# Kernel tuning notes

Hardware: AMD Instinct MI355X
Metric: run time of the kernel (lower is better)

Reference implementation:

```python
import jax, jax.numpy as jnp
import numpy as np

D_MODEL = 1024
N_HEADS = 16
HEAD_DIM = D_MODEL // N_HEADS
BATCH = 2
SEQ = 2048


def setup_inputs() -> dict:
    key = jax.random.key(0)
    ks = jax.random.split(key, 7)
    s = 1.0 / np.sqrt(D_MODEL)
    return {
        "x": jax.random.normal(ks[0], (BATCH, SEQ, D_MODEL), dtype=jnp.float32),
        "Wq": jax.random.normal(ks[1], (D_MODEL, D_MODEL), dtype=jnp.float32) * s,
        "Wk": jax.random.normal(ks[2], (D_MODEL, D_MODEL), dtype=jnp.float32) * s,
        "Wv": jax.random.normal(ks[3], (D_MODEL, D_MODEL), dtype=jnp.float32) * s,
        "Wo": jax.random.normal(ks[4], (D_MODEL, D_MODEL), dtype=jnp.float32) * s,
        "Wg": jax.random.normal(ks[5], (D_MODEL, D_MODEL), dtype=jnp.float32) * s,
        "bg": jnp.zeros((D_MODEL,), dtype=jnp.float32),
    }


def _rope_cos_sin(seq_len, head_dim, dtype):
    half = head_dim // 2
    inv_freq = 1.0 / (10000.0 ** (jnp.arange(half, dtype=jnp.float32) / half))
    freqs = jnp.arange(seq_len, dtype=jnp.float32)[:, None] * inv_freq[None, :]  # (S, half)
    emb = jnp.concatenate([freqs, freqs], axis=-1)  # (S, head_dim)
    return jnp.cos(emb).astype(dtype), jnp.sin(emb).astype(dtype)


def _rotate_half(x):
    half = x.shape[-1] // 2
    return jnp.concatenate([-x[..., half:], x[..., :half]], axis=-1)


def reference(x, Wq, Wk, Wv, Wo, Wg, bg):
    bsz, seq_len, d_model = x.shape
    # projections (torch Linear: x @ W.T)
    q = jnp.einsum('bsd,ed->bse', x, Wq).reshape(bsz, seq_len, N_HEADS, HEAD_DIM).transpose(0, 2, 1, 3)
    k = jnp.einsum('bsd,ed->bse', x, Wk).reshape(bsz, seq_len, N_HEADS, HEAD_DIM).transpose(0, 2, 1, 3)
    v = jnp.einsum('bsd,ed->bse', x, Wv).reshape(bsz, seq_len, N_HEADS, HEAD_DIM).transpose(0, 2, 1, 3)
    cos, sin = _rope_cos_sin(seq_len, HEAD_DIM, x.dtype)  # (S, hd)
    cos = cos[None, None]
    sin = sin[None, None]
    q = q * cos + _rotate_half(q) * sin
    k = k * cos + _rotate_half(k) * sin
    scores = jnp.einsum('bhqd,bhkd->bhqk', q, k) / jnp.sqrt(jnp.asarray(HEAD_DIM, x.dtype))
    causal = jnp.triu(jnp.full((seq_len, seq_len), -jnp.inf, dtype=x.dtype), k=1)
    scores = scores + causal
    probs = jax.nn.softmax(scores, axis=-1)
    attn = jnp.einsum('bhqk,bhkd->bhqd', probs, v)  # (B,H,S,hd)
    attn = attn.transpose(0, 2, 1, 3).reshape(bsz, seq_len, d_model)
    out = jnp.einsum('bsd,ed->bse', attn, Wo)
    gate = jax.nn.sigmoid(jnp.einsum('bsd,ed->bse', out, Wg) + bg)
    return out * gate
```

## Files before the change

### kernel.cpp

```cpp
#include <hip/hip_runtime.h>

#define DM 1024
#define NH 16
#define HD 64
#define BATCH 2
#define SEQ 2048
#define MROWS (BATCH*SEQ)

typedef unsigned short u16;
typedef unsigned long long u64;
typedef __bf16 bf16x8 __attribute__((ext_vector_type(8)));
typedef float f32x4 __attribute__((ext_vector_type(4)));
typedef unsigned int u32x4 __attribute__((ext_vector_type(4)));
typedef unsigned int __attribute__((address_space(1))) as1_uint;
typedef unsigned int __attribute__((address_space(3))) as3_uint;

__device__ __forceinline__ u16 f2bf(float f) {
  unsigned u = __builtin_bit_cast(unsigned, f);
  u += 0x7fffu + ((u >> 16) & 1u);
  return (u16)(u >> 16);
}
__device__ __forceinline__ float bf2f(u16 h) {
  return __builtin_bit_cast(float, ((unsigned)h) << 16);
}
__device__ __forceinline__ bf16x8 ld8(const u16* p) {
  return __builtin_bit_cast(bf16x8, *reinterpret_cast<const u32x4*>(p));
}
__device__ __forceinline__ void gl_lds16(const u16* g, void* lds) {
  __builtin_amdgcn_global_load_lds((const as1_uint*)(const void*)g,
                                   (as3_uint*)lds, 16, 0, 0);
}
__device__ __forceinline__ unsigned pk2(float a, float b) {
  return __builtin_amdgcn_perm(__builtin_bit_cast(unsigned, a),
                               __builtin_bit_cast(unsigned, b), 0x07060302u);
}

__global__ void convall_kernel(const float* __restrict__ x,
                               const float* __restrict__ w0, const float* __restrict__ w1,
                               const float* __restrict__ w2, const float* __restrict__ w3,
                               const float* __restrict__ w4, u16* __restrict__ out) {
  const size_t NX = (size_t)MROWS * DM;
  size_t i = ((size_t)blockIdx.x * 256 + threadIdx.x) * 4;
  const float* src;
  size_t off;
  if (i < NX) { src = x; off = i; }
  else {
    size_t j = i - NX;
    int wsel = (int)(j >> 20);
    off = j & ((1u << 20) - 1);
    src = (wsel == 0) ? w0 : (wsel == 1) ? w1 : (wsel == 2) ? w2 : (wsel == 3) ? w3 : w4;
  }
  f32x4 v = *reinterpret_cast<const f32x4*>(src + off);
  out[i + 0] = f2bf(v[0]);
  out[i + 1] = f2bf(v[1]);
  out[i + 2] = f2bf(v[2]);
  out[i + 3] = f2bf(v[3]);
}

__global__ void tab_kernel(float* __restrict__ tab) {
  int t = blockIdx.x * 256 + threadIdx.x;
  if (t >= SEQ * 32) return;
  int s = t >> 5, i = t & 31;
  float inv = powf(10000.0f, -(float)i / 32.0f);
  float f = (float)s * inv;
  tab[s * 64 + i] = cosf(f);
  tab[s * 64 + 32 + i] = sinf(f);
}

template <int MODE>
__global__ __launch_bounds__(256) void gemm_bt(
    const u16* __restrict__ A, const u16* __restrict__ B,
    u16* __restrict__ Cbf, float* __restrict__ Cf,
    const float* __restrict__ bias, const float* __restrict__ mult,
    int M, int N, int K, size_t bz, size_t cz) {
  B += blockIdx.z * bz;
  u16* Cb = Cbf + blockIdx.z * cz;
  const int gx = gridDim.x;
  {
    int nwg = gx * gridDim.y;
    int flat = blockIdx.y * gx + blockIdx.x;
    flat = (flat & 7) * (nwg >> 3) + (flat >> 3);
    const int bx = flat % gx, by = flat / gx;
    A += (size_t)by * 128 * K;
    B += (size_t)bx * 64 * K;
    Cb += (size_t)by * 128 * N + bx * 64;
    if constexpr (MODE != 0) Cf += (size_t)by * 128 * N + bx * 64;
    if constexpr (MODE == 2) { bias += bx * 64; mult += (size_t)by * 128 * N + bx * 64; }
  }
  const int t = threadIdx.x, w = t >> 6;
  const int l = t & 63;
  const int wr = w >> 1, wc = w & 1;
  const int lr = l & 15, lg = l >> 4;
  __shared__ __align__(16) u16 As[128 * 32];
  __shared__ __align__(16) u16 Bs[64 * 32];
  f32x4 acc[4][2] = {};
  const int srow = t >> 2;
  const int sc8 = (t & 3) * 8;
  const u16* gA = A + (size_t)srow * K + sc8;
  const u16* gB = B + (size_t)srow * K + sc8;
  char* lA = (char*)As + w * 1024;
  char* lB = (char*)Bs + w * 1024;
  const size_t rstep = (size_t)64 * K;

  for (int kt = 0; kt < K; kt += 32) {
    gl_lds16(gA + kt, lA);
    gl_lds16(gA + kt + rstep, lA + 4096);
    gl_lds16(gB + kt, lB);
    __syncthreads();
    bf16x8 af[4], bfr[2];
#pragma unroll
    for (int i = 0; i < 4; ++i)
      af[i] = ld8(&As[(wr * 64 + i * 16 + lr) * 32 + lg * 8]);
#pragma unroll
    for (int i = 0; i < 2; ++i)
      bfr[i] = ld8(&Bs[(wc * 32 + i * 16 + lr) * 32 + lg * 8]);
#pragma unroll
    for (int mi = 0; mi < 4; ++mi)
#pragma unroll
      for (int ni = 0; ni < 2; ++ni)
        acc[mi][ni] = __builtin_amdgcn_mfma_f32_16x16x32_bf16(af[mi], bfr[ni], acc[mi][ni], 0, 0, 0);
    __syncthreads();
  }
#pragma unroll
  for (int mi = 0; mi < 4; ++mi)
#pragma unroll
    for (int ni = 0; ni < 2; ++ni)
#pragma unroll
      for (int r = 0; r < 4; ++r) {
        int row = wr * 64 + mi * 16 + lg * 4 + r;
        int col = wc * 32 + ni * 16 + lr;
        size_t idx = (size_t)row * N + col;
        float v = acc[mi][ni][r];
        if constexpr (MODE == 0) {
          Cb[idx] = f2bf(v);
        } else if constexpr (MODE == 1) {
          Cf[idx] = v;
          Cb[idx] = f2bf(v);
        } else {
          float g = 1.0f / (1.0f + __expf(-(v + bias[col])));
          Cf[idx] = mult[idx] * g;
        }
      }
}

__global__ void rope_kernel(const u16* __restrict__ Qin, const u16* __restrict__ Kin,
                            u16* __restrict__ Qr, u16* __restrict__ Kr,
                            const float* __restrict__ tab) {
  int t = blockIdx.x * 256 + threadIdx.x;
  int i = t & 31;
  int s = (t >> 5) & (SEQ - 1);
  int bh = t >> 16;
  if (bh >= BATCH * NH) return;
  int b = bh >> 4, h = bh & 15;
  size_t ib = ((size_t)(b * SEQ + s)) * DM + h * 64;
  size_t ob = ((size_t)bh * SEQ + s) * 64;
  float c = tab[s * 64 + i], sn = tab[s * 64 + 32 + i];
  float q1 = bf2f(Qin[ib + i]), q2 = bf2f(Qin[ib + 32 + i]);
  float k1 = bf2f(Kin[ib + i]), k2 = bf2f(Kin[ib + 32 + i]);
  Qr[ob + i] = f2bf(q1 * c - q2 * sn);
  Qr[ob + 32 + i] = f2bf(q2 * c + q1 * sn);
  Kr[ob + i] = f2bf(k1 * c - k2 * sn);
  Kr[ob + 32 + i] = f2bf(k2 * c + k1 * sn);
}

__global__ __launch_bounds__(256) void vtrans_kernel(const u16* __restrict__ Vin,
                                                     u16* __restrict__ Vt) {
  const int s0 = blockIdx.x * 64;
  const int bh = blockIdx.y;
  const int b = bh >> 4, h = bh & 15;
  const int t = threadIdx.x;
  __shared__ __align__(16) u16 T[64][72];
  const int row = t >> 3, col = (t & 7) * 8;
#pragma unroll
  for (int p = 0; p < 2; ++p) {
    int r = p * 32 + row;
    *reinterpret_cast<u32x4*>(&T[r][col]) =
        *reinterpret_cast<const u32x4*>(&Vin[(size_t)(b * SEQ + s0 + r) * DM + h * 64 + col]);
  }
  __syncthreads();
  const size_t ob = (size_t)bh * 64 * SEQ;
#pragma unroll
  for (int p = 0; p < 2; ++p) {
    int dr = p * 32 + row;
    u16 tmp[8];
#pragma unroll
    for (int j = 0; j < 8; ++j) tmp[j] = T[col + j][dr];
    *reinterpret_cast<u32x4*>(&Vt[ob + (size_t)dr * SEQ + s0 + col]) =
        *reinterpret_cast<u32x4*>(tmp);
  }
}

__global__ __launch_bounds__(256) void attn_kernel(
    const u16* __restrict__ Q, const u16* __restrict__ K, const u16* __restrict__ Vt,
    u16* __restrict__ O) {
  const int qb_raw = blockIdx.x;
  const int bh_raw = blockIdx.y;
  const int xs = qb_raw & 7, hi = qb_raw >> 3;
  const int lo = bh_raw & 15, rr = bh_raw >> 4;
  const int bh = xs * 4 + (lo & 3);
  const int q0i = hi + 2 * (lo >> 2);
  const int qb = rr ? (15 - q0i) : q0i;

  const int t = threadIdx.x, w = t >> 6, l = t & 63;
  const int lr = l & 15, lg = l >> 4;
  const int qw0 = qb * 128 + w * 32;
  const size_t base = (size_t)bh * SEQ * 64;
  const size_t vbase = (size_t)bh * 64 * SEQ;
  __shared__ __align__(16) u16 Ks[2][64 * 64];
  __shared__ __align__(16) u16 Vs[2][64 * 64];
  __shared__ __align__(16) u16 Ps[4][2][1024];

  bf16x8 qf[2][2];
#pragma unroll
  for (int qs = 0; qs < 2; ++qs) {
    const u16* qp = &Q[base + (size_t)(qw0 + qs * 16 + lr) * 64 + lg * 8];
    qf[qs][0] = ld8(qp);
    qf[qs][1] = ld8(qp + 32);
  }

  f32x4 oacc[2][4] = {};
  float l_run[2] = {0.0f, 0.0f};

  const int nt = (qb + 1) * 2;
  const int srow = t >> 3, sc16 = t & 7;
  const int lo0 = srow * 128 + ((sc16 * 16) ^ ((srow & 7) << 4));
  const int lo1 = lo0 + 4096;
  const u16* Kg = K + base + sc16 * 8;
  const u16* Vg = Vt + vbase + sc16 * 8;
  u32x4 rg[4];

#define LOADG(tile) do { const int kv_ = (tile) * 64;                     \
    rg[0] = *(const u32x4*)(Kg + (size_t)(kv_ + srow) * 64);              \
    rg[1] = *(const u32x4*)(Kg + (size_t)(kv_ + srow + 32) * 64);         \
    rg[2] = *(const u32x4*)(Vg + (size_t)srow * SEQ + kv_);               \
    rg[3] = *(const u32x4*)(Vg + (size_t)(srow + 32) * SEQ + kv_); } while (0)

#define WRITEL(tile) do { char* kb_ = (char*)Ks[(tile) & 1];              \
    char* vb_ = (char*)Vs[(tile) & 1];                                    \
    *(u32x4*)(kb_ + lo0) = rg[0]; *(u32x4*)(kb_ + lo1) = rg[1];           \
    *(u32x4*)(vb_ + lo0) = rg[2]; *(u32x4*)(vb_ + lo1) = rg[3]; } while (0)

  LOADG(0);
  WRITEL(0);
  __syncthreads();

  for (int tk = 0; tk < nt; ++tk) {
    const int cur = tk & 1;
    const int kv0 = tk * 64;
    if (tk + 1 < nt) LOADG(tk + 1);
    const char* kb = (const char*)Ks[cur];
    const char* vb = (const char*)Vs[cur];
    if (kv0 <= qw0 + 31) {
      bf16x8 kf[4][2];
      const int swk = (lr & 7) << 4;
#pragma unroll
      for (int h = 0; h < 4; ++h) {
        const char* rp = kb + (h * 16 + lr) * 128;
        kf[h][0] = *(const bf16x8*)(rp + ((lg * 16) ^ swk));
        kf[h][1] = *(const bf16x8*)(rp + ((64 + lg * 16) ^ swk));
      }
      const int qslo = (kv0 <= qw0 + 15) ? 0 : 1;
      const int swz = (lr & 7) << 4;
#pragma unroll
      for (int qs = 0; qs < 2; ++qs) {
        if (qs < qslo) continue;
        const int qs0 = qw0 + qs * 16;
        f32x4 st[4];
#pragma unroll
        for (int h = 0; h < 4; ++h) {
          f32x4 z = {};
          z = __builtin_amdgcn_mfma_f32_16x16x32_bf16(kf[h][0], qf[qs][0], z, 0, 0, 0);
          z = __builtin_amdgcn_mfma_f32_16x16x32_bf16(kf[h][1], qf[qs][1], z, 0, 0, 0);
          st[h] = z;
        }
        float pv[4][4];
#pragma unroll
        for (int h = 0; h < 4; ++h)
#pragma unroll
          for (int r = 0; r < 4; ++r)
            pv[h][r] = fmaf(st[h][r], 0.1803368801f, -12.0f);
        if (kv0 + 63 > qs0) {
#pragma unroll
          for (int h = 0; h < 4; ++h)
#pragma unroll
            for (int r = 0; r < 4; ++r)
              if (kv0 + h * 16 + lg * 4 + r > qs0 + lr) pv[h][r] = -1e30f;
        }
        float hs[4];
#pragma unroll
        for (int h = 0; h < 4; ++h) {
#pragma unroll
          for (int r = 0; r < 4; ++r) pv[h][r] = exp2f(pv[h][r]);
          hs[h] = (pv[h][0] + pv[h][1]) + (pv[h][2] + pv[h][3]);
        }
        float ts = (hs[0] + hs[1]) + (hs[2] + hs[3]);
        ts += __shfl_xor(ts, 16);
        ts += __shfl_xor(ts, 32);
        l_run[qs] += ts;
        char* pq = (char*)Ps[w][qs];
#pragma unroll
        for (int h = 0; h < 4; ++h) {
          u64 pw = (u64)pk2(pv[h][1], pv[h][0]) | ((u64)pk2(pv[h][3], pv[h][2]) << 32);
          *(u64*)(pq + ((((h >> 1) * 512 + lr * 32 + (h & 1) * 16 + lg * 4) * 2) ^ swz)) = pw;
        }
      }
#pragma unroll
      for (int ks = 0; ks < 2; ++ks) {
        bf16x8 pf[2];
#pragma unroll
        for (int qs = 0; qs < 2; ++qs)
          if (qs >= qslo)
            pf[qs] = *(const bf16x8*)((char*)Ps[w][qs] +
                                      ((ks * 1024 + lr * 64 + lg * 16) ^ swz));
#pragma unroll
        for (int dc = 0; dc < 4; ++dc) {
          const int row = dc * 16 + lr;
          bf16x8 vf = *(const bf16x8*)(vb + row * 128 +
                                       (((ks * 64) + lg * 16) ^ ((lr & 7) << 4)));
#pragma unroll
          for (int qs = 0; qs < 2; ++qs)
            if (qs >= qslo)
              oacc[qs][dc] = __builtin_amdgcn_mfma_f32_16x16x32_bf16(pf[qs], vf, oacc[qs][dc], 0, 0, 0);
        }
      }
    }
    if (tk + 1 < nt) {
      WRITEL(tk + 1);
      __syncthreads();
    }
  }
#undef LOADG
#undef WRITEL
  const int b = bh >> 4, hh = bh & 15;
#pragma unroll
  for (int qs = 0; qs < 2; ++qs) {
    const int qs0 = qw0 + qs * 16;
#pragma unroll
    for (int r = 0; r < 4; ++r) {
      float inv = 1.0f / __shfl(l_run[qs], lg * 4 + r);
#pragma unroll
      for (int dc = 0; dc < 4; ++dc)
        O[((size_t)(b * SEQ + qs0 + lg * 4 + r)) * DM + hh * 64 + dc * 16 + lr] =
            f2bf(oacc[qs][dc][r] * inv);
    }
  }
}

extern "C" void kernel_launch(void* const* d_in, const int* in_sizes, int n_in,
                              void* d_out, int out_size, void* d_ws, size_t ws_size,
                              hipStream_t stream) {
  const float* x = (const float*)d_in[0];
  const float* Wq = (const float*)d_in[1];
  const float* Wk = (const float*)d_in[2];
  const float* Wv = (const float*)d_in[3];
  const float* Wo = (const float*)d_in[4];
  const float* Wg = (const float*)d_in[5];
  const float* bg = (const float*)d_in[6];
  float* out = (float*)d_out;

  const size_t NX = (size_t)MROWS * DM;
  const size_t NW = (size_t)DM * DM;
  u16* xbf = (u16*)d_ws;
  u16* wbf = xbf + NX;
  u16* qkv = wbf + 5 * NW;
  u16* qkvr = qkv + 3 * NX;
  u16* attn = qkvr + 3 * NX;
  u16* outbf = attn + NX;
  float* outf = (float*)(outbf + NX);
  float* tab = outf + NX;

  convall_kernel<<<(NX + 5 * NW) / 1024, 256, 0, stream>>>(x, Wq, Wk, Wv, Wo, Wg, xbf);
  tab_kernel<<<(SEQ * 32) / 256, 256, 0, stream>>>(tab);
  gemm_bt<0><<<dim3(DM / 64, MROWS / 128, 3), 256, 0, stream>>>(
      xbf, wbf, qkv, nullptr, nullptr, nullptr, MROWS, DM, DM, NW, NX);
  rope_kernel<<<(BATCH * NH * SEQ * 32) / 256, 256, 0, stream>>>(
      qkv, qkv + NX, qkvr, qkvr + NX, tab);
  vtrans_kernel<<<dim3(SEQ / 64, BATCH * NH), 256, 0, stream>>>(
      qkv + 2 * NX, qkvr + 2 * NX);
  attn_kernel<<<dim3(SEQ / 128, BATCH * NH), 256, 0, stream>>>(
      qkvr, qkvr + NX, qkvr + 2 * NX, attn);
  gemm_bt<1><<<dim3(DM / 64, MROWS / 128, 1), 256, 0, stream>>>(
      attn, wbf + 3 * NW, outbf, outf, nullptr, nullptr, MROWS, DM, DM, 0, 0);
  gemm_bt<2><<<dim3(DM / 64, MROWS / 128, 1), 256, 0, stream>>>(
      outbf, wbf + 4 * NW, nullptr, out, bg, outf, MROWS, DM, DM, 0, 0);
}
```

Measured before the change: 251.7 us.

## Fuse RoPE and V transpose into QKV GEMM, restructure attention kernel

Replaces the separate QKV GEMM, RoPE, and V-transpose kernels with one GEMM whose epilogue applies RoPE to Q/K and writes V transposed through shared memory. This removes two extra passes over the QKV intermediates and two launches. The attention kernel moves to 128-thread blocks over 64-row query tiles with a new load-balanced tile order. K is staged via direct global-to-LDS loads, V fragments are read straight from global memory, and the per-tile row-sum shuffles are deferred to the end. The gating GEMM now reads the bf16 output instead of a separate fp32 copy, which drops an fp32 write and read but slightly lowers precision of the multiplier.

After: 239.1 us. 5.0% less time.

```diff
diff --git a/kernel.cpp b/kernel.cpp
--- a/kernel.cpp
+++ b/kernel.cpp
@@ -67,25 +67,107 @@
   tab[s * 64 + 32 + i] = sinf(f);
 }
 
+__global__ __launch_bounds__(256) void qkv_gemm(
+    const u16* __restrict__ A, const u16* __restrict__ Bw,
+    u16* __restrict__ Qr, u16* __restrict__ Kr, u16* __restrict__ Vt,
+    const float* __restrict__ tab) {
+  const int z = blockIdx.z;
+  const u16* B = Bw + (size_t)z * DM * DM;
+  int flat = blockIdx.y * 16 + blockIdx.x;
+  flat = (flat & 7) * 64 + (flat >> 3);
+  const int bx = flat & 15, by = flat >> 4;
+  const int m0 = by * 128;
+  const int h = bx;
+  const int t = threadIdx.x, w = t >> 6, l = t & 63;
+  const int lr = l & 15, lg = l >> 4;
+  __shared__ __align__(16) u16 SM[8704];
+  u16* As = SM;
+  u16* Bs = SM + 4096;
+  f32x4 acc[2][4] = {};
+  const int srow = t >> 2, sc8 = (t & 3) * 8;
+  const u16* gA = A + (size_t)(m0 + srow) * DM + sc8;
+  const u16* gB = B + (size_t)(h * 64 + srow) * DM + sc8;
+  char* lA = (char*)As + w * 1024;
+  char* lB = (char*)Bs + w * 1024;
+  const size_t rstep = (size_t)64 * DM;
+
+  for (int kt = 0; kt < DM; kt += 32) {
+    gl_lds16(gA + kt, lA);
+    gl_lds16(gA + kt + rstep, lA + 4096);
+    gl_lds16(gB + kt, lB);
+    __syncthreads();
+    bf16x8 af[2], bfr[4];
+    af[0] = ld8(&As[(w * 32 + lr) * 32 + lg * 8]);
+    af[1] = ld8(&As[(w * 32 + 16 + lr) * 32 + lg * 8]);
+#pragma unroll
+    for (int ni = 0; ni < 4; ++ni) bfr[ni] = ld8(&Bs[(ni * 16 + lr) * 32 + lg * 8]);
+#pragma unroll
+    for (int mi = 0; mi < 2; ++mi)
+#pragma unroll
+      for (int ni = 0; ni < 4; ++ni)
+        acc[mi][ni] = __builtin_amdgcn_mfma_f32_16x16x32_bf16(af[mi], bfr[ni], acc[mi][ni], 0, 0, 0);
+    __syncthreads();
+  }
+
+  if (z < 2) {
+    u16* Out = (z == 0) ? Qr : Kr;
+#pragma unroll
+    for (int mi = 0; mi < 2; ++mi)
+#pragma unroll
+      for (int r = 0; r < 4; ++r) {
+        const int row = m0 + w * 32 + mi * 16 + lg * 4 + r;
+        const int b = row >> 11, s = row & (SEQ - 1);
+        const size_t ob = ((size_t)(b * NH + h) * SEQ + s) * 64;
+#pragma unroll
+        for (int ni = 0; ni < 2; ++ni) {
+          const int i = ni * 16 + lr;
+          const float c = tab[s * 64 + i], sn = tab[s * 64 + 32 + i];
+          const float v1 = acc[mi][ni][r], v2 = acc[mi][ni + 2][r];
+          Out[ob + i] = f2bf(v1 * c - v2 * sn);
+          Out[ob + 32 + i] = f2bf(v2 * c + v1 * sn);
+        }
+      }
+  } else {
+    u16* T = SM;
+#pragma unroll
+    for (int mi = 0; mi < 2; ++mi)
+#pragma unroll
+      for (int ni = 0; ni < 4; ++ni) {
+        const int cc = ni * 16 + lr;
+        const int rw = w * 32 + mi * 16 + lg * 4;
+#pragma unroll
+        for (int r = 0; r < 4; ++r) T[cc * 136 + rw + r] = f2bf(acc[mi][ni][r]);
+      }
+    __syncthreads();
+    const int d = t >> 2, seg = t & 3;
+    const int b = m0 >> 11, sbase = (m0 & (SEQ - 1)) + seg * 32;
+    u16* dst = Vt + ((size_t)(b * NH + h) * 64 + d) * SEQ + sbase;
+    const u16* srcT = T + d * 136 + seg * 32;
+#pragma unroll
+    for (int j = 0; j < 4; ++j)
+      *reinterpret_cast<u32x4*>(dst + j * 8) =
+          *reinterpret_cast<const u32x4*>(srcT + j * 8);
+  }
+}
+
 template <int MODE>
 __global__ __launch_bounds__(256) void gemm_bt(
     const u16* __restrict__ A, const u16* __restrict__ B,
-    u16* __restrict__ Cbf, float* __restrict__ Cf,
-    const float* __restrict__ bias, const float* __restrict__ mult,
-    int M, int N, int K, size_t bz, size_t cz) {
-  B += blockIdx.z * bz;
-  u16* Cb = Cbf + blockIdx.z * cz;
+    u16* __restrict__ Cb, float* __restrict__ Cf,
+    const float* __restrict__ bias, const u16* __restrict__ mult,
+    int M, int N, int K) {
   const int gx = gridDim.x;
-  {
-    int nwg = gx * gridDim.y;
-    int flat = blockIdx.y * gx + blockIdx.x;
-    flat = (flat & 7) * (nwg >> 3) + (flat >> 3);
-    const int bx = flat % gx, by = flat / gx;
-    A += (size_t)by * 128 * K;
-    B += (size_t)bx * 64 * K;
-    Cb += (size_t)by * 128 * N + bx * 64;
-    if constexpr (MODE != 0) Cf += (size_t)by * 128 * N + bx * 64;
-    if constexpr (MODE == 2) { bias += bx * 64; mult += (size_t)by * 128 * N + bx * 64; }
+  int nwg = gx * gridDim.y;
+  int flat = blockIdx.y * gx + blockIdx.x;
+  flat = (flat & 7) * (nwg >> 3) + (flat >> 3);
+  const int bx = flat % gx, by = flat / gx;
+  A += (size_t)by * 128 * K;
+  B += (size_t)bx * 64 * K;
+  if constexpr (MODE == 1) Cb += (size_t)by * 128 * N + bx * 64;
+  if constexpr (MODE == 2) {
+    Cf += (size_t)by * 128 * N + bx * 64;
+    bias += bx * 64;
+    mult += (size_t)by * 128 * N + bx * 64;
   }
   const int t = threadIdx.x, w = t >> 6;
   const int l = t & 63;
@@ -131,84 +213,32 @@
         int col = wc * 32 + ni * 16 + lr;
         size_t idx = (size_t)row * N + col;
         float v = acc[mi][ni][r];
-        if constexpr (MODE == 0) {
-          Cb[idx] = f2bf(v);
-        } else if constexpr (MODE == 1) {
-          Cf[idx] = v;
+        if constexpr (MODE == 1) {
           Cb[idx] = f2bf(v);
         } else {
           float g = 1.0f / (1.0f + __expf(-(v + bias[col])));
-          Cf[idx] = mult[idx] * g;
+          Cf[idx] = bf2f(mult[idx]) * g;
         }
       }
 }
 
-__global__ void rope_kernel(const u16* __restrict__ Qin, const u16* __restrict__ Kin,
-                            u16* __restrict__ Qr, u16* __restrict__ Kr,
-                            const float* __restrict__ tab) {
-  int t = blockIdx.x * 256 + threadIdx.x;
-  int i = t & 31;
-  int s = (t >> 5) & (SEQ - 1);
-  int bh = t >> 16;
-  if (bh >= BATCH * NH) return;
-  int b = bh >> 4, h = bh & 15;
-  size_t ib = ((size_t)(b * SEQ + s)) * DM + h * 64;
-  size_t ob = ((size_t)bh * SEQ + s) * 64;
-  float c = tab[s * 64 + i], sn = tab[s * 64 + 32 + i];
-  float q1 = bf2f(Qin[ib + i]), q2 = bf2f(Qin[ib + 32 + i]);
-  float k1 = bf2f(Kin[ib + i]), k2 = bf2f(Kin[ib + 32 + i]);
-  Qr[ob + i] = f2bf(q1 * c - q2 * sn);
-  Qr[ob + 32 + i] = f2bf(q2 * c + q1 * sn);
-  Kr[ob + i] = f2bf(k1 * c - k2 * sn);
-  Kr[ob + 32 + i] = f2bf(k2 * c + k1 * sn);
-}
-
-__global__ __launch_bounds__(256) void vtrans_kernel(const u16* __restrict__ Vin,
-                                                     u16* __restrict__ Vt) {
-  const int s0 = blockIdx.x * 64;
-  const int bh = blockIdx.y;
-  const int b = bh >> 4, h = bh & 15;
-  const int t = threadIdx.x;
-  __shared__ __align__(16) u16 T[64][72];
-  const int row = t >> 3, col = (t & 7) * 8;
-#pragma unroll
-  for (int p = 0; p < 2; ++p) {
-    int r = p * 32 + row;
-    *reinterpret_cast<u32x4*>(&T[r][col]) =
-        *reinterpret_cast<const u32x4*>(&Vin[(size_t)(b * SEQ + s0 + r) * DM + h * 64 + col]);
-  }
-  __syncthreads();
-  const size_t ob = (size_t)bh * 64 * SEQ;
-#pragma unroll
-  for (int p = 0; p < 2; ++p) {
-    int dr = p * 32 + row;
-    u16 tmp[8];
-#pragma unroll
-    for (int j = 0; j < 8; ++j) tmp[j] = T[col + j][dr];
-    *reinterpret_cast<u32x4*>(&Vt[ob + (size_t)dr * SEQ + s0 + col]) =
-        *reinterpret_cast<u32x4*>(tmp);
-  }
-}
-
-__global__ __launch_bounds__(256) void attn_kernel(
+__global__ __launch_bounds__(128) void attn_kernel(
     const u16* __restrict__ Q, const u16* __restrict__ K, const u16* __restrict__ Vt,
     u16* __restrict__ O) {
-  const int qb_raw = blockIdx.x;
-  const int bh_raw = blockIdx.y;
-  const int xs = qb_raw & 7, hi = qb_raw >> 3;
-  const int lo = bh_raw & 15, rr = bh_raw >> 4;
-  const int bh = xs * 4 + (lo & 3);
-  const int q0i = hi + 2 * (lo >> 2);
-  const int qb = rr ? (15 - q0i) : q0i;
+  const int f = blockIdx.x;
+  const int rank = f >> 3;
+  const int bh = (f & 7) * 4 + (rank & 3);
+  const int j = rank >> 2;
+  const int u = j & 7, v = j >> 3;
+  const int qb = (v == 0) ? (31 - u) : (v == 1) ? (16 + u) : (v == 2) ? (15 - u) : u;
 
   const int t = threadIdx.x, w = t >> 6, l = t & 63;
   const int lr = l & 15, lg = l >> 4;
-  const int qw0 = qb * 128 + w * 32;
+  const int qw0 = qb * 64 + w * 32;
   const size_t base = (size_t)bh * SEQ * 64;
   const size_t vbase = (size_t)bh * 64 * SEQ;
   __shared__ __align__(16) u16 Ks[2][64 * 64];
-  __shared__ __align__(16) u16 Vs[2][64 * 64];
-  __shared__ __align__(16) u16 Ps[4][2][1024];
+  __shared__ __align__(16) u16 Ps[2][2][1024];
 
   bf16x8 qf[2][2];
 #pragma unroll
@@ -219,125 +249,104 @@
   }
 
   f32x4 oacc[2][4] = {};
-  float l_run[2] = {0.0f, 0.0f};
-
-  const int nt = (qb + 1) * 2;
-  const int srow = t >> 3, sc16 = t & 7;
-  const int lo0 = srow * 128 + ((sc16 * 16) ^ ((srow & 7) << 4));
-  const int lo1 = lo0 + 4096;
-  const u16* Kg = K + base + sc16 * 8;
-  const u16* Vg = Vt + vbase + sc16 * 8;
-  u32x4 rg[4];
-
-#define LOADG(tile) do { const int kv_ = (tile) * 64;                     \
-    rg[0] = *(const u32x4*)(Kg + (size_t)(kv_ + srow) * 64);              \
-    rg[1] = *(const u32x4*)(Kg + (size_t)(kv_ + srow + 32) * 64);         \
-    rg[2] = *(const u32x4*)(Vg + (size_t)srow * SEQ + kv_);               \
-    rg[3] = *(const u32x4*)(Vg + (size_t)(srow + 32) * SEQ + kv_); } while (0)
-
-#define WRITEL(tile) do { char* kb_ = (char*)Ks[(tile) & 1];              \
-    char* vb_ = (char*)Vs[(tile) & 1];                                    \
-    *(u32x4*)(kb_ + lo0) = rg[0]; *(u32x4*)(kb_ + lo1) = rg[1];           \
-    *(u32x4*)(vb_ + lo0) = rg[2]; *(u32x4*)(vb_ + lo1) = rg[3]; } while (0)
-
-  LOADG(0);
-  WRITEL(0);
+  float l_part[2] = {0.0f, 0.0f};
+  const int nt = qb + 1;
+
+#define STAGE_K(tile) do { const int kv_ = (tile) * 64; u16* kb_ = Ks[(tile) & 1];   \
+    _Pragma("unroll") for (int c_ = 0; c_ < 4; ++c_) {                               \
+      const int row_ = w * 32 + c_ * 8 + (l >> 3);                                   \
+      const int slot_ = (l & 7) ^ (row_ & 7);                                        \
+      gl_lds16(K + base + (size_t)(kv_ + row_) * 64 + slot_ * 8,                     \
+               (char*)kb_ + (w * 32 + c_ * 8) * 128);                                \
+    } } while (0)
+
+  STAGE_K(0);
   __syncthreads();
 
   for (int tk = 0; tk < nt; ++tk) {
-    const int cur = tk & 1;
     const int kv0 = tk * 64;
-    if (tk + 1 < nt) LOADG(tk + 1);
-    const char* kb = (const char*)Ks[cur];
-    const char* vb = (const char*)Vs[cur];
-    if (kv0 <= qw0 + 31) {
-      bf16x8 kf[4][2];
-      const int swk = (lr & 7) << 4;
+    const char* kb = (const char*)Ks[tk & 1];
+    bf16x8 vf[2][4];
+#pragma unroll
+    for (int ks = 0; ks < 2; ++ks)
+#pragma unroll
+      for (int dc = 0; dc < 4; ++dc)
+        vf[ks][dc] = ld8(&Vt[vbase + (size_t)(dc * 16 + lr) * SEQ + kv0 + ks * 32 + lg * 8]);
+    if (tk + 1 < nt) STAGE_K(tk + 1);
+
+    bf16x8 kf[4][2];
+    const int swk = lr & 7;
+#pragma unroll
+    for (int h = 0; h < 4; ++h) {
+      const char* rp = kb + (h * 16 + lr) * 128;
+      kf[h][0] = *(const bf16x8*)(rp + ((lg ^ swk) << 4));
+      kf[h][1] = *(const bf16x8*)(rp + (((4 + lg) ^ swk) << 4));
+    }
+    const int swz = (lr & 7) << 4;
+#pragma unroll
+    for (int qs = 0; qs < 2; ++qs) {
+      const int qs0 = qw0 + qs * 16;
+      f32x4 st[4];
 #pragma unroll
       for (int h = 0; h < 4; ++h) {
-        const char* rp = kb + (h * 16 + lr) * 128;
-        kf[h][0] = *(const bf16x8*)(rp + ((lg * 16) ^ swk));
-        kf[h][1] = *(const bf16x8*)(rp + ((64 + lg * 16) ^ swk));
-      }
-      const int qslo = (kv0 <= qw0 + 15) ? 0 : 1;
-      const int swz = (lr & 7) << 4;
-#pragma unroll
-      for (int qs = 0; qs < 2; ++qs) {
-        if (qs < qslo) continue;
-        const int qs0 = qw0 + qs * 16;
-        f32x4 st[4];
-#pragma unroll
-        for (int h = 0; h < 4; ++h) {
-          f32x4 z = {};
-          z = __builtin_amdgcn_mfma_f32_16x16x32_bf16(kf[h][0], qf[qs][0], z, 0, 0, 0);
-          z = __builtin_amdgcn_mfma_f32_16x16x32_bf16(kf[h][1], qf[qs][1], z, 0, 0, 0);
-          st[h] = z;
-        }
-        float pv[4][4];
+        f32x4 z = {};
+        z = __builtin_amdgcn_mfma_f32_16x16x32_bf16(kf[h][0], qf[qs][0], z, 0, 0, 0);
+        z = __builtin_amdgcn_mfma_f32_16x16x32_bf16(kf[h][1], qf[qs][1], z, 0, 0, 0);
+        st[h] = z;
+      }
+      float pv[4][4];
+#pragma unroll
+      for (int h = 0; h < 4; ++h)
+#pragma unroll
+        for (int r = 0; r < 4; ++r)
+          pv[h][r] = fmaf(st[h][r], 0.1803368801f, -12.0f);
+      if (tk == qb) {
 #pragma unroll
         for (int h = 0; h < 4; ++h)
 #pragma unroll
           for (int r = 0; r < 4; ++r)
-            pv[h][r] = fmaf(st[h][r], 0.1803368801f, -12.0f);
-        if (kv0 + 63 > qs0) {
-#pragma unroll
-          for (int h = 0; h < 4; ++h)
-#pragma unroll
-            for (int r = 0; r < 4; ++r)
-              if (kv0 + h * 16 + lg * 4 + r > qs0 + lr) pv[h][r] = -1e30f;
-        }
-        float hs[4];
-#pragma unroll
-        for (int h = 0; h < 4; ++h) {
-#pragma unroll
-          for (int r = 0; r < 4; ++r) pv[h][r] = exp2f(pv[h][r]);
-          hs[h] = (pv[h][0] + pv[h][1]) + (pv[h][2] + pv[h][3]);
-        }
-        float ts = (hs[0] + hs[1]) + (hs[2] + hs[3]);
-        ts += __shfl_xor(ts, 16);
-        ts += __shfl_xor(ts, 32);
-        l_run[qs] += ts;
-        char* pq = (char*)Ps[w][qs];
-#pragma unroll
-        for (int h = 0; h < 4; ++h) {
-          u64 pw = (u64)pk2(pv[h][1], pv[h][0]) | ((u64)pk2(pv[h][3], pv[h][2]) << 32);
-          *(u64*)(pq + ((((h >> 1) * 512 + lr * 32 + (h & 1) * 16 + lg * 4) * 2) ^ swz)) = pw;
-        }
-      }
-#pragma unroll
-      for (int ks = 0; ks < 2; ++ks) {
-        bf16x8 pf[2];
+            if (kv0 + h * 16 + lg * 4 + r > qs0 + lr) pv[h][r] = -1e30f;
+      }
+      float hs[4];
+#pragma unroll
+      for (int h = 0; h < 4; ++h) {
+#pragma unroll
+        for (int r = 0; r < 4; ++r) pv[h][r] = exp2f(pv[h][r]);
+        hs[h] = (pv[h][0] + pv[h][1]) + (pv[h][2] + pv[h][3]);
+      }
+      l_part[qs] += (hs[0] + hs[1]) + (hs[2] + hs[3]);
+      char* pq = (char*)Ps[w][qs];
+#pragma unroll
+      for (int h = 0; h < 4; ++h) {
+        u64 pw = (u64)pk2(pv[h][1], pv[h][0]) | ((u64)pk2(pv[h][3], pv[h][2]) << 32);
+        *(u64*)(pq + ((((h >> 1) * 512 + lr * 32 + (h & 1) * 16 + lg * 4) * 2) ^ swz)) = pw;
+      }
+    }
+#pragma unroll
+    for (int ks = 0; ks < 2; ++ks) {
+      bf16x8 pf[2];
+#pragma unroll
+      for (int qs = 0; qs < 2; ++qs)
+        pf[qs] = *(const bf16x8*)((char*)Ps[w][qs] + ((ks * 1024 + lr * 64 + lg * 16) ^ swz));
+#pragma unroll
+      for (int dc = 0; dc < 4; ++dc)
 #pragma unroll
         for (int qs = 0; qs < 2; ++qs)
-          if (qs >= qslo)
-            pf[qs] = *(const bf16x8*)((char*)Ps[w][qs] +
-                                      ((ks * 1024 + lr * 64 + lg * 16) ^ swz));
-#pragma unroll
-        for (int dc = 0; dc < 4; ++dc) {
-          const int row = dc * 16 + lr;
-          bf16x8 vf = *(const bf16x8*)(vb + row * 128 +
-                                       (((ks * 64) + lg * 16) ^ ((lr & 7) << 4)));
-#pragma unroll
-          for (int qs = 0; qs < 2; ++qs)
-            if (qs >= qslo)
-              oacc[qs][dc] = __builtin_amdgcn_mfma_f32_16x16x32_bf16(pf[qs], vf, oacc[qs][dc], 0, 0, 0);
-        }
-      }
+          oacc[qs][dc] = __builtin_amdgcn_mfma_f32_16x16x32_bf16(pf[qs], vf[ks][dc], oacc[qs][dc], 0, 0, 0);
     }
-    if (tk + 1 < nt) {
-      WRITEL(tk + 1);
-      __syncthreads();
-    }
-  }
-#undef LOADG
-#undef WRITEL
+    __syncthreads();
+  }
+#undef STAGE_K
   const int b = bh >> 4, hh = bh & 15;
 #pragma unroll
   for (int qs = 0; qs < 2; ++qs) {
+    float ls = l_part[qs];
+    ls += __shfl_xor(ls, 16);
+    ls += __shfl_xor(ls, 32);
     const int qs0 = qw0 + qs * 16;
 #pragma unroll
     for (int r = 0; r < 4; ++r) {
-      float inv = 1.0f / __shfl(l_run[qs], lg * 4 + r);
+      float inv = 1.0f / __shfl(ls, lg * 4 + r);
 #pragma unroll
       for (int dc = 0; dc < 4; ++dc)
         O[((size_t)(b * SEQ + qs0 + lg * 4 + r)) * DM + hh * 64 + dc * 16 + lr] =
@@ -362,25 +371,19 @@
   const size_t NW = (size_t)DM * DM;
   u16* xbf = (u16*)d_ws;
   u16* wbf = xbf + NX;
-  u16* qkv = wbf + 5 * NW;
-  u16* qkvr = qkv + 3 * NX;
+  u16* qkvr = wbf + 5 * NW;
   u16* attn = qkvr + 3 * NX;
   u16* outbf = attn + NX;
-  float* outf = (float*)(outbf + NX);
-  float* tab = outf + NX;
+  float* tab = (float*)(outbf + NX);
 
   convall_kernel<<<(NX + 5 * NW) / 1024, 256, 0, stream>>>(x, Wq, Wk, Wv, Wo, Wg, xbf);
   tab_kernel<<<(SEQ * 32) / 256, 256, 0, stream>>>(tab);
-  gemm_bt<0><<<dim3(DM / 64, MROWS / 128, 3), 256, 0, stream>>>(
-      xbf, wbf, qkv, nullptr, nullptr, nullptr, MROWS, DM, DM, NW, NX);
-  rope_kernel<<<(BATCH * NH * SEQ * 32) / 256, 256, 0, stream>>>(
-      qkv, qkv + NX, qkvr, qkvr + NX, tab);
-  vtrans_kernel<<<dim3(SEQ / 64, BATCH * NH), 256, 0, stream>>>(
-      qkv + 2 * NX, qkvr + 2 * NX);
-  attn_kernel<<<dim3(SEQ / 128, BATCH * NH), 256, 0, stream>>>(
+  qkv_gemm<<<dim3(16, 32, 3), 256, 0, stream>>>(
+      xbf, wbf, qkvr, qkvr + NX, qkvr + 2 * NX, tab);
+  attn_kernel<<<dim3(1024), 128, 0, stream>>>(
       qkvr, qkvr + NX, qkvr + 2 * NX, attn);
-  gemm_bt<1><<<dim3(DM / 64, MROWS / 128, 1), 256, 0, stream>>>(
-      attn, wbf + 3 * NW, outbf, outf, nullptr, nullptr, MROWS, DM, DM, 0, 0);
-  gemm_bt<2><<<dim3(DM / 64, MROWS / 128, 1), 256, 0, stream>>>(
-      outbf, wbf + 4 * NW, nullptr, out, bg, outf, MROWS, DM, DM, 0, 0);
-}
+  gemm_bt<1><<<dim3(16, 32), 256, 0, stream>>>(
+      attn, wbf + 3 * NW, outbf, nullptr, nullptr, nullptr, MROWS, DM, DM);
+  gemm_bt<2><<<dim3(16, 32), 256, 0, stream>>>(
+      outbf, wbf + 4 * NW, nullptr, out, bg, outbf, MROWS, DM, DM);
+}
```
